# Kernel tuning notes

Hardware: AMD Instinct MI355X
Metric: run time of the kernel (lower is better)

The kernel has to match this reference:

```python
import math
import jax, jax.numpy as jnp
import numpy as np

NUM_HEADS = 16
QUERY_SIZE = 1024
SEQ = 2048
HEAD = QUERY_SIZE // NUM_HEADS  # qk_size = vo_size = 64


def setup_inputs() -> dict:
    key = jax.random.key(0)
    ks = jax.random.split(key, 8)
    s = 0.02
    query = jax.random.normal(ks[0], (SEQ, QUERY_SIZE), jnp.float32)
    key_ = jax.random.normal(ks[1], (SEQ, QUERY_SIZE), jnp.float32)
    value = jax.random.normal(ks[2], (SEQ, QUERY_SIZE), jnp.float32)
    # causal mask (mask='causal' with state=None -> offset 0)
    mask = jnp.tril(jnp.ones((SEQ, SEQ), dtype=bool))
    Wq = jax.random.normal(ks[3], (QUERY_SIZE, QUERY_SIZE), jnp.float32) * s
    Wk = jax.random.normal(ks[4], (QUERY_SIZE, QUERY_SIZE), jnp.float32) * s
    Wv = jax.random.normal(ks[5], (QUERY_SIZE, QUERY_SIZE), jnp.float32) * s
    Wo = jax.random.normal(ks[6], (QUERY_SIZE, QUERY_SIZE), jnp.float32) * s
    return {"query": query, "key_": key_, "value": value, "mask": mask,
            "Wq": Wq, "Wk": Wk, "Wv": Wv, "Wo": Wo}


def reference(query, key_, value, mask, Wq, Wk, Wv, Wo):
    H, D = NUMS = NUM_HEADS, HEAD
    S = query.shape[0]
    inv_sqrt_d = 1.0 / math.sqrt(D)
    # per-token linear projections, split into heads: [S, H, D]
    q = (query @ Wq.T).reshape(S, H, D)
    k = (key_ @ Wk.T).reshape(S, H, D)
    v = (value @ Wv.T).reshape(S, H, D)
    # NOTE: original divides BOTH q and k by sqrt(d) (effective 1/d scaling)
    q = q * inv_sqrt_d
    k = k * inv_sqrt_d
    # logits per head: [H, S, S]
    logits = jnp.einsum('shd,Shd->hsS', q, k)
    logits = jnp.where(mask[None, :, :], logits, jnp.finfo(logits.dtype).min)
    # per-head GLOBAL max subtraction, softmax in fp32, cast back (faithful)
    m = jnp.max(logits, axis=(1, 2), keepdims=True)
    weights = jax.nn.softmax((logits - m).astype(jnp.float32), axis=-1).astype(query.dtype)
    attn = jnp.einsum('hsS,ShD->shD', weights, v).reshape(S, H * D)
    return attn @ Wo.T
```

## Files before the change

### kernel.cpp

```cpp
#include <hip/hip_runtime.h>
#include <hip/hip_bf16.h>

typedef __bf16 bf16_t;
typedef __bf16 bf16x8 __attribute__((ext_vector_type(8)));
typedef float f32x4 __attribute__((ext_vector_type(4)));

#define MFMA(A, B, C) __builtin_amdgcn_mfma_f32_16x16x32_bf16(A, B, C, 0, 0, 0)

#define GLL16(g, l) __builtin_amdgcn_global_load_lds(                      \
    (const __attribute__((address_space(1))) void*)(g),                    \
    (__attribute__((address_space(3))) void*)(l), 16, 0, 0)

__global__ __launch_bounds__(256) void cvt_all(
    const float* __restrict__ q, const float* __restrict__ k, const float* __restrict__ v,
    const float* __restrict__ wq, const float* __restrict__ wk,
    const float* __restrict__ wv, const float* __restrict__ wo,
    bf16_t* __restrict__ xq, bf16_t* __restrict__ xk, bf16_t* __restrict__ xv,
    bf16_t* __restrict__ ywq, bf16_t* __restrict__ ywk,
    bf16_t* __restrict__ ywv, bf16_t* __restrict__ ywo)
{
  const long gid = (long)blockIdx.x * 256 + threadIdx.x;
  const float* s; bf16_t* d; long off; float sc = 1.0f;
  if (gid < 262144)       { s = q;  d = xq;  off = gid; }
  else if (gid < 524288)  { s = k;  d = xk;  off = gid - 262144; }
  else if (gid < 786432)  { s = v;  d = xv;  off = gid - 524288; }
  else if (gid < 917504)  { s = wq; d = ywq; off = gid - 786432;  sc = 0.125f; }
  else if (gid < 1048576) { s = wk; d = ywk; off = gid - 917504;  sc = 0.125f; }
  else if (gid < 1179648) { s = wv; d = ywv; off = gid - 1048576; }
  else                    { s = wo; d = ywo; off = gid - 1179648; }
  const float* p = s + off * 8;
  float4 a = *(const float4*)p, b = *(const float4*)(p + 4);
  bf16x8 o;
  o[0] = (bf16_t)(a.x * sc); o[1] = (bf16_t)(a.y * sc);
  o[2] = (bf16_t)(a.z * sc); o[3] = (bf16_t)(a.w * sc);
  o[4] = (bf16_t)(b.x * sc); o[5] = (bf16_t)(b.y * sc);
  o[6] = (bf16_t)(b.z * sc); o[7] = (bf16_t)(b.w * sc);
  *(bf16x8*)(d + off * 8) = o;
}

__device__ __forceinline__ void gemm_core(const bf16_t* __restrict__ A,
                                          const bf16_t* __restrict__ W,
                                          int bm, int bn,
                                          bf16_t (&As)[2][128 * 64],
                                          bf16_t (&Bs)[2][64 * 64],
                                          f32x4 (&acc)[4][2])
{
  const int tid = threadIdx.x, lane = tid & 63, wave = tid >> 6;
  const int l15 = lane & 15, l4 = lane >> 4, l7 = l15 & 7;
  const int wm = (wave >> 1) * 64, wn = (wave & 1) * 32;

  auto stage = [&](int buf, int k0) {
#pragma unroll
    for (int i = 0; i < 4; ++i) {
      const int id = i * 256 + tid;
      const int row = id >> 3, cph = id & 7;
      GLL16(A + (size_t)(bm + row) * 1024 + k0 + 8 * (cph ^ (row & 7)),
            &As[buf][(i * 256 + wave * 64) * 8]);
    }
#pragma unroll
    for (int i = 0; i < 2; ++i) {
      const int id = i * 256 + tid;
      const int row = id >> 3, cph = id & 7;
      GLL16(W + (size_t)(bn + row) * 1024 + k0 + 8 * (cph ^ (row & 7)),
            &Bs[buf][(i * 256 + wave * 64) * 8]);
    }
  };

  stage(0, 0);
#pragma unroll
  for (int s = 0; s < 16; ++s) {
    if (s + 1 < 16) stage((s + 1) & 1, (s + 1) * 64);
    __syncthreads();
    const bf16_t* as = As[s & 1];
    const bf16_t* bs = Bs[s & 1];
#pragma unroll
    for (int ks = 0; ks < 2; ++ks) {
      bf16x8 af[4], bfr[2];
#pragma unroll
      for (int i = 0; i < 4; ++i)
        af[i] = *(const bf16x8*)(&as[(wm + i * 16 + l15) * 64 + 8 * ((ks * 4 + l4) ^ l7)]);
#pragma unroll
      for (int j = 0; j < 2; ++j)
        bfr[j] = *(const bf16x8*)(&bs[(wn + j * 16 + l15) * 64 + 8 * ((ks * 4 + l4) ^ l7)]);
#pragma unroll
      for (int i = 0; i < 4; ++i)
#pragma unroll
        for (int j = 0; j < 2; ++j)
          acc[i][j] = MFMA(af[i], bfr[j], acc[i][j]);
    }
    __syncthreads();
  }
}

__global__ __launch_bounds__(256) void gemm_qkv(
    const bf16_t* __restrict__ xq, const bf16_t* __restrict__ xk, const bf16_t* __restrict__ xv,
    const bf16_t* __restrict__ ywq, const bf16_t* __restrict__ ywk, const bf16_t* __restrict__ ywv,
    bf16_t* __restrict__ qo, bf16_t* __restrict__ ko, bf16_t* __restrict__ vt)
{
  __shared__ __align__(16) bf16_t As[2][128 * 64];
  __shared__ __align__(16) bf16_t Bs[2][64 * 64];
  const int z = blockIdx.z;
  const bf16_t* A = z == 0 ? xq : z == 1 ? xk : xv;
  const bf16_t* W = z == 0 ? ywq : z == 1 ? ywk : ywv;
  const int bm = blockIdx.x * 128, bn = blockIdx.y * 64;
  f32x4 acc[4][2] = {};
  gemm_core(A, W, bm, bn, As, Bs, acc);
  const int tid = threadIdx.x, lane = tid & 63, wave = tid >> 6;
  const int l15 = lane & 15, l4 = lane >> 4;
  const int wm = (wave >> 1) * 64, wn = (wave & 1) * 32;
  if (z < 2) {
    bf16_t* C = z == 0 ? qo : ko;
#pragma unroll
    for (int i = 0; i < 4; ++i)
#pragma unroll
      for (int j = 0; j < 2; ++j)
#pragma unroll
        for (int r = 0; r < 4; ++r)
          C[(size_t)(bm + wm + i * 16 + 4 * l4 + r) * 1024 + bn + wn + j * 16 + l15] =
              (bf16_t)acc[i][j][r];
  } else {
#pragma unroll
    for (int i = 0; i < 4; ++i)
#pragma unroll
      for (int j = 0; j < 2; ++j)
#pragma unroll
        for (int r = 0; r < 4; ++r)
          vt[(size_t)(bn + wn + j * 16 + l15) * 2048 + bm + wm + i * 16 + 4 * l4 + r] =
              (bf16_t)acc[i][j][r];
  }
}

__global__ __launch_bounds__(256) void gemm_out(
    const bf16_t* __restrict__ ctx, const bf16_t* __restrict__ ywo, float* __restrict__ out)
{
  __shared__ __align__(16) bf16_t As[2][128 * 64];
  __shared__ __align__(16) bf16_t Bs[2][64 * 64];
  const int bm = blockIdx.x * 128, bn = blockIdx.y * 64;
  f32x4 acc[4][2] = {};
  gemm_core(ctx, ywo, bm, bn, As, Bs, acc);
  const int tid = threadIdx.x, lane = tid & 63, wave = tid >> 6;
  const int l15 = lane & 15, l4 = lane >> 4;
  const int wm = (wave >> 1) * 64, wn = (wave & 1) * 32;
#pragma unroll
  for (int i = 0; i < 4; ++i)
#pragma unroll
    for (int j = 0; j < 2; ++j)
#pragma unroll
      for (int r = 0; r < 4; ++r)
        out[(size_t)(bm + wm + i * 16 + 4 * l4 + r) * 1024 + bn + wn + j * 16 + l15] =
            acc[i][j][r];
}

__global__ __launch_bounds__(512) void attn512(
    const bf16_t* __restrict__ Qb, const bf16_t* __restrict__ Kb,
    const bf16_t* __restrict__ Vt, bf16_t* __restrict__ Ctx)
{
  __shared__ __align__(16) bf16_t Ks[2][128 * 64];
  __shared__ __align__(16) bf16_t Vs[2][64 * 128];
  __shared__ __align__(16) bf16_t Ps[8][16 * 64];

  const int bid = blockIdx.x;
  const int h = 2 * (bid & 7) + ((bid >> 3) >> 4);
  const int jp = (bid >> 3) & 15;
  const int hoff = h * 64;
  const int tid = threadIdx.x;
  const int lane = tid & 63, wave = tid >> 6;
  const int g = wave & 3, kh = wave >> 2;
  const int l15 = lane & 15, l4 = lane >> 4;
  const int l7 = l15 & 7;

  const int qtA = jp, qtB = 31 - jp;
  const int qbA = qtA * 64, qbB = qtB * 64;
  const int nscA = qtA / 2 + 1, nscB = qtB / 2 + 1;

  const int qrA = qbA + g * 16 + l15, qrB = qbB + g * 16 + l15;
  bf16x8 qA0 = *(const bf16x8*)(Qb + (size_t)qrA * 1024 + hoff + 8 * l4);
  bf16x8 qA1 = *(const bf16x8*)(Qb + (size_t)qrA * 1024 + hoff + 32 + 8 * l4);
  bf16x8 qB0 = *(const bf16x8*)(Qb + (size_t)qrB * 1024 + hoff + 8 * l4);
  bf16x8 qB1 = *(const bf16x8*)(Qb + (size_t)qrB * 1024 + hoff + 32 + 8 * l4);

  f32x4 oA[4] = {}, oB[4] = {};
  float dA[4] = {0.f, 0.f, 0.f, 0.f}, dB[4] = {0.f, 0.f, 0.f, 0.f};

  bf16x8 rk[2], rv[2];
  auto issue = [&](int sc) {
    const int t0 = sc * 128;
#pragma unroll
    for (int i = 0; i < 2; ++i) {
      const int id = tid + 512 * i;
      const int kr = id >> 3, kc = id & 7;
      rk[i] = *(const bf16x8*)(Kb + (size_t)(t0 + kr) * 1024 + hoff + 8 * kc);
      const int vr = id >> 4, vc = id & 15;
      rv[i] = *(const bf16x8*)(Vt + (size_t)(hoff + vr) * 2048 + t0 + 8 * vc);
    }
  };
  auto commit = [&](int buf) {
#pragma unroll
    for (int i = 0; i < 2; ++i) {
      const int id = tid + 512 * i;
      const int kr = id >> 3, kc = id & 7;
      *(bf16x8*)(&Ks[buf][kr * 64 + 8 * (kc ^ (kr & 7))]) = rk[i];
      const int vr = id >> 4, vc = id & 15;
      *(bf16x8*)(&Vs[buf][vr * 128 + 8 * (vc ^ (vr & 7))]) = rv[i];
    }
  };

  auto process = [&](int sc, int cur, int qb, const bf16x8& q0, const bf16x8& q1,
                     f32x4 (&oacc)[4], float (&den)[4]) {
    if (128 * sc + 64 * kh > qb + g * 16 + 15) return;
    const int tb = 128 * sc + 64 * kh;
#pragma unroll
    for (int sub = 0; sub < 4; ++sub) {
      const int krow = 64 * kh + 16 * sub + l15;
      bf16x8 kf0 = *(const bf16x8*)(&Ks[cur][krow * 64 + 8 * (l4 ^ l7)]);
      bf16x8 kf1 = *(const bf16x8*)(&Ks[cur][krow * 64 + 8 * ((4 + l4) ^ l7)]);
      f32x4 sv = {};
      sv = MFMA(q0, kf0, sv);
      sv = MFMA(q1, kf1, sv);
      const int t = tb + 16 * sub + l15;
#pragma unroll
      for (int r = 0; r < 4; ++r) {
        const int qq = qb + g * 16 + 4 * l4 + r;
        const float p = (t <= qq) ? __expf(sv[r]) : 0.0f;
        const bf16_t pb = (bf16_t)p;
        den[r] += (float)pb;
        const int prow = 4 * l4 + r;
        const int pch = 2 * sub + (l15 >> 3);
        Ps[wave][prow * 64 + 8 * (pch ^ (prow & 7)) + l7] = pb;
      }
    }
    asm volatile("s_waitcnt lgkmcnt(0)" ::: "memory");
#pragma unroll
    for (int ks = 0; ks < 2; ++ks) {
      bf16x8 pf = *(const bf16x8*)(&Ps[wave][l15 * 64 + 8 * ((ks * 4 + l4) ^ l7)]);
#pragma unroll
      for (int db = 0; db < 4; ++db) {
        bf16x8 vf = *(const bf16x8*)(&Vs[cur][(db * 16 + l15) * 128 + 64 * kh + 8 * ((ks * 4 + l4) ^ l7)]);
        oacc[db] = MFMA(pf, vf, oacc[db]);
      }
    }
  };

  issue(0);
  commit(0);
  int cur = 0;
  for (int sc = 0; sc < nscB; ++sc) {
    const bool pre = (sc + 1 < nscB);
    if (pre) issue(sc + 1);
    __syncthreads();
    process(sc, cur, qbB, qB0, qB1, oB, dB);
    if (sc < nscA) process(sc, cur, qbA, qA0, qA1, oA, dA);
    if (pre) commit(cur ^ 1);
    cur ^= 1;
  }

  __syncthreads();
#pragma unroll
  for (int r = 0; r < 4; ++r)
#pragma unroll
    for (int m = 1; m < 16; m <<= 1) {
      dA[r] += __shfl_xor(dA[r], m, 64);
      dB[r] += __shfl_xor(dB[r], m, 64);
    }
  float* Os = (float*)(&Ks[0][0]);
  float* Ds = (float*)(&Vs[0][0]);
  if (kh == 1) {
#pragma unroll
    for (int r = 0; r < 4; ++r) {
      const int row = g * 16 + 4 * l4 + r;
#pragma unroll
      for (int db = 0; db < 4; ++db) {
        Os[(0 * 64 + row) * 64 + db * 16 + l15] = oA[db][r];
        Os[(1 * 64 + row) * 64 + db * 16 + l15] = oB[db][r];
      }
      if (l15 == 0) { Ds[0 * 64 + row] = dA[r]; Ds[1 * 64 + row] = dB[r]; }
    }
  }
  __syncthreads();
  if (kh == 0) {
#pragma unroll
    for (int r = 0; r < 4; ++r) {
      const int row = g * 16 + 4 * l4 + r;
      const float iA = 1.0f / (dA[r] + Ds[0 * 64 + row]);
      const float iB = 1.0f / (dB[r] + Ds[1 * 64 + row]);
#pragma unroll
      for (int db = 0; db < 4; ++db) {
        const float vA = oA[db][r] + Os[(0 * 64 + row) * 64 + db * 16 + l15];
        const float vB = oB[db][r] + Os[(1 * 64 + row) * 64 + db * 16 + l15];
        Ctx[(size_t)(qbA + row) * 1024 + hoff + db * 16 + l15] = (bf16_t)(vA * iA);
        Ctx[(size_t)(qbB + row) * 1024 + hoff + db * 16 + l15] = (bf16_t)(vB * iB);
      }
    }
  }
}

extern "C" void kernel_launch(void* const* d_in, const int* in_sizes, int n_in,
                              void* d_out, int out_size, void* d_ws, size_t ws_size,
                              hipStream_t stream)
{
  const float* query = (const float*)d_in[0];
  const float* key_  = (const float*)d_in[1];
  const float* value = (const float*)d_in[2];
  const float* Wq = (const float*)d_in[4];
  const float* Wk = (const float*)d_in[5];
  const float* Wv = (const float*)d_in[6];
  const float* Wo = (const float*)d_in[7];
  float* out = (float*)d_out;

  const size_t SE = (size_t)2048 * 1024, EE = (size_t)1024 * 1024;
  bf16_t* xq  = (bf16_t*)d_ws;
  bf16_t* xk  = xq + SE;
  bf16_t* xv  = xk + SE;
  bf16_t* wq  = xv + SE;
  bf16_t* wk  = wq + EE;
  bf16_t* wv  = wk + EE;
  bf16_t* wo  = wv + EE;
  bf16_t* qo  = wo + EE;
  bf16_t* ko  = qo + SE;
  bf16_t* vt  = ko + SE;
  bf16_t* ctx = vt + SE;

  cvt_all<<<5120, 256, 0, stream>>>(query, key_, value, Wq, Wk, Wv, Wo,
                                    xq, xk, xv, wq, wk, wv, wo);
  gemm_qkv<<<dim3(16, 16, 3), 256, 0, stream>>>(xq, xk, xv, wq, wk, wv, qo, ko, vt);
  attn512<<<256, 512, 0, stream>>>(qo, ko, vt, ctx);
  gemm_out<<<dim3(16, 16), 256, 0, stream>>>(ctx, wo, out);
}
```

Baseline: 72.08 us.

## Fuse fp32-to-bf16 conversion into GEMM loaders and add MFMA priority hints

Removes the separate conversion kernel. Both GEMMs now load fp32 activations and weights straight into registers, convert to bf16 (applying the 1/8 scale to Wq and Wk) and write swizzled tiles into LDS through a register-staged double buffer. This saves one kernel launch and a bf16 workspace round trip. The cost is that each GEMM now reads twice the global bytes and does its own conversions, and the GEMMs re-read the weights from every block. The attention kernel also gets s_setprio boosts around its MFMA sections, and its barrier moves ahead of the prefetch issue.

```diff
diff --git a/kernel.cpp b/kernel.cpp
--- a/kernel.cpp
+++ b/kernel.cpp
@@ -11,103 +11,91 @@
     (const __attribute__((address_space(1))) void*)(g),                    \
     (__attribute__((address_space(3))) void*)(l), 16, 0, 0)
 
-__global__ __launch_bounds__(256) void cvt_all(
-    const float* __restrict__ q, const float* __restrict__ k, const float* __restrict__ v,
-    const float* __restrict__ wq, const float* __restrict__ wk,
-    const float* __restrict__ wv, const float* __restrict__ wo,
-    bf16_t* __restrict__ xq, bf16_t* __restrict__ xk, bf16_t* __restrict__ xv,
-    bf16_t* __restrict__ ywq, bf16_t* __restrict__ ywk,
-    bf16_t* __restrict__ ywv, bf16_t* __restrict__ ywo)
-{
-  const long gid = (long)blockIdx.x * 256 + threadIdx.x;
-  const float* s; bf16_t* d; long off; float sc = 1.0f;
-  if (gid < 262144)       { s = q;  d = xq;  off = gid; }
-  else if (gid < 524288)  { s = k;  d = xk;  off = gid - 262144; }
-  else if (gid < 786432)  { s = v;  d = xv;  off = gid - 524288; }
-  else if (gid < 917504)  { s = wq; d = ywq; off = gid - 786432;  sc = 0.125f; }
-  else if (gid < 1048576) { s = wk; d = ywk; off = gid - 917504;  sc = 0.125f; }
-  else if (gid < 1179648) { s = wv; d = ywv; off = gid - 1048576; }
-  else                    { s = wo; d = ywo; off = gid - 1179648; }
-  const float* p = s + off * 8;
-  float4 a = *(const float4*)p, b = *(const float4*)(p + 4);
+static __device__ __forceinline__ bf16x8 cvt8p(const float4& a, const float4& b, float sc) {
   bf16x8 o;
   o[0] = (bf16_t)(a.x * sc); o[1] = (bf16_t)(a.y * sc);
   o[2] = (bf16_t)(a.z * sc); o[3] = (bf16_t)(a.w * sc);
   o[4] = (bf16_t)(b.x * sc); o[5] = (bf16_t)(b.y * sc);
   o[6] = (bf16_t)(b.z * sc); o[7] = (bf16_t)(b.w * sc);
-  *(bf16x8*)(d + off * 8) = o;
-}
-
-__device__ __forceinline__ void gemm_core(const bf16_t* __restrict__ A,
-                                          const bf16_t* __restrict__ W,
-                                          int bm, int bn,
-                                          bf16_t (&As)[2][128 * 64],
-                                          bf16_t (&Bs)[2][64 * 64],
-                                          f32x4 (&acc)[4][2])
-{
-  const int tid = threadIdx.x, lane = tid & 63, wave = tid >> 6;
-  const int l15 = lane & 15, l4 = lane >> 4, l7 = l15 & 7;
-  const int wm = (wave >> 1) * 64, wn = (wave & 1) * 32;
-
-  auto stage = [&](int buf, int k0) {
-#pragma unroll
-    for (int i = 0; i < 4; ++i) {
-      const int id = i * 256 + tid;
-      const int row = id >> 3, cph = id & 7;
-      GLL16(A + (size_t)(bm + row) * 1024 + k0 + 8 * (cph ^ (row & 7)),
-            &As[buf][(i * 256 + wave * 64) * 8]);
-    }
-#pragma unroll
-    for (int i = 0; i < 2; ++i) {
-      const int id = i * 256 + tid;
-      const int row = id >> 3, cph = id & 7;
-      GLL16(W + (size_t)(bn + row) * 1024 + k0 + 8 * (cph ^ (row & 7)),
-            &Bs[buf][(i * 256 + wave * 64) * 8]);
-    }
-  };
-
-  stage(0, 0);
-#pragma unroll
-  for (int s = 0; s < 16; ++s) {
-    if (s + 1 < 16) stage((s + 1) & 1, (s + 1) * 64);
-    __syncthreads();
-    const bf16_t* as = As[s & 1];
-    const bf16_t* bs = Bs[s & 1];
-#pragma unroll
-    for (int ks = 0; ks < 2; ++ks) {
-      bf16x8 af[4], bfr[2];
-#pragma unroll
-      for (int i = 0; i < 4; ++i)
-        af[i] = *(const bf16x8*)(&as[(wm + i * 16 + l15) * 64 + 8 * ((ks * 4 + l4) ^ l7)]);
-#pragma unroll
-      for (int j = 0; j < 2; ++j)
-        bfr[j] = *(const bf16x8*)(&bs[(wn + j * 16 + l15) * 64 + 8 * ((ks * 4 + l4) ^ l7)]);
-#pragma unroll
-      for (int i = 0; i < 4; ++i)
-#pragma unroll
-        for (int j = 0; j < 2; ++j)
-          acc[i][j] = MFMA(af[i], bfr[j], acc[i][j]);
-    }
-    __syncthreads();
-  }
+  return o;
 }
 
 __global__ __launch_bounds__(256) void gemm_qkv(
-    const bf16_t* __restrict__ xq, const bf16_t* __restrict__ xk, const bf16_t* __restrict__ xv,
-    const bf16_t* __restrict__ ywq, const bf16_t* __restrict__ ywk, const bf16_t* __restrict__ ywv,
+    const float* __restrict__ xq, const float* __restrict__ xk, const float* __restrict__ xv,
+    const float* __restrict__ Wq, const float* __restrict__ Wk, const float* __restrict__ Wv,
     bf16_t* __restrict__ qo, bf16_t* __restrict__ ko, bf16_t* __restrict__ vt)
 {
   __shared__ __align__(16) bf16_t As[2][128 * 64];
   __shared__ __align__(16) bf16_t Bs[2][64 * 64];
   const int z = blockIdx.z;
-  const bf16_t* A = z == 0 ? xq : z == 1 ? xk : xv;
-  const bf16_t* W = z == 0 ? ywq : z == 1 ? ywk : ywv;
+  const float* A = z == 0 ? xq : z == 1 ? xk : xv;
+  const float* W = z == 0 ? Wq : z == 1 ? Wk : Wv;
+  const float wsc = z < 2 ? 0.125f : 1.0f;
   const int bm = blockIdx.x * 128, bn = blockIdx.y * 64;
+  const int tid = threadIdx.x, lane = tid & 63, wave = tid >> 6;
+  const int l15 = lane & 15, l4 = lane >> 4, l7 = l15 & 7;
+  const int wm = (wave >> 1) * 64, wn = (wave & 1) * 32;
+
+  float4 ra[4][2], rb[2][2];
+  auto aload = [&](int k0) {
+#pragma unroll
+    for (int i = 0; i < 4; ++i) {
+      const int id = i * 256 + tid, row = id >> 3, c = id & 7;
+      const float* p = A + (size_t)(bm + row) * 1024 + k0 + 8 * c;
+      ra[i][0] = *(const float4*)p; ra[i][1] = *(const float4*)(p + 4);
+    }
+  };
+  auto bload = [&](int k0) {
+#pragma unroll
+    for (int i = 0; i < 2; ++i) {
+      const int id = i * 256 + tid, row = id >> 3, c = id & 7;
+      const float* p = W + (size_t)(bn + row) * 1024 + k0 + 8 * c;
+      rb[i][0] = *(const float4*)p; rb[i][1] = *(const float4*)(p + 4);
+    }
+  };
+  auto abwrite = [&](int buf) {
+#pragma unroll
+    for (int i = 0; i < 4; ++i) {
+      const int id = i * 256 + tid, row = id >> 3, c = id & 7;
+      *(bf16x8*)(&As[buf][row * 64 + 8 * (c ^ (row & 7))]) = cvt8p(ra[i][0], ra[i][1], 1.0f);
+    }
+#pragma unroll
+    for (int i = 0; i < 2; ++i) {
+      const int id = i * 256 + tid, row = id >> 3, c = id & 7;
+      *(bf16x8*)(&Bs[buf][row * 64 + 8 * (c ^ (row & 7))]) = cvt8p(rb[i][0], rb[i][1], wsc);
+    }
+  };
+
   f32x4 acc[4][2] = {};
-  gemm_core(A, W, bm, bn, As, Bs, acc);
-  const int tid = threadIdx.x, lane = tid & 63, wave = tid >> 6;
-  const int l15 = lane & 15, l4 = lane >> 4;
-  const int wm = (wave >> 1) * 64, wn = (wave & 1) * 32;
+  aload(0); bload(0);
+  abwrite(0);
+  aload(64); bload(64);
+#pragma unroll
+  for (int s = 0; s < 16; ++s) {
+    __syncthreads();
+    if (s + 1 < 16) {
+      abwrite((s + 1) & 1);
+      if (s + 2 < 16) { aload((s + 2) * 64); bload((s + 2) * 64); }
+    }
+    const bf16_t* as = As[s & 1];
+    const bf16_t* bs = Bs[s & 1];
+#pragma unroll
+    for (int ks = 0; ks < 2; ++ks) {
+      bf16x8 af[4], bfr[2];
+#pragma unroll
+      for (int i = 0; i < 4; ++i)
+        af[i] = *(const bf16x8*)(&as[(wm + i * 16 + l15) * 64 + 8 * ((ks * 4 + l4) ^ l7)]);
+#pragma unroll
+      for (int j = 0; j < 2; ++j)
+        bfr[j] = *(const bf16x8*)(&bs[(wn + j * 16 + l15) * 64 + 8 * ((ks * 4 + l4) ^ l7)]);
+#pragma unroll
+      for (int i = 0; i < 4; ++i)
+#pragma unroll
+        for (int j = 0; j < 2; ++j)
+          acc[i][j] = MFMA(af[i], bfr[j], acc[i][j]);
+    }
+  }
+
   if (z < 2) {
     bf16_t* C = z == 0 ? qo : ko;
 #pragma unroll
@@ -131,16 +119,70 @@
 }
 
 __global__ __launch_bounds__(256) void gemm_out(
-    const bf16_t* __restrict__ ctx, const bf16_t* __restrict__ ywo, float* __restrict__ out)
+    const bf16_t* __restrict__ ctx, const float* __restrict__ Wo, float* __restrict__ out)
 {
   __shared__ __align__(16) bf16_t As[2][128 * 64];
   __shared__ __align__(16) bf16_t Bs[2][64 * 64];
   const int bm = blockIdx.x * 128, bn = blockIdx.y * 64;
+  const int tid = threadIdx.x, lane = tid & 63, wave = tid >> 6;
+  const int l15 = lane & 15, l4 = lane >> 4, l7 = l15 & 7;
+  const int wm = (wave >> 1) * 64, wn = (wave & 1) * 32;
+
+  auto astage = [&](int buf, int k0) {
+#pragma unroll
+    for (int i = 0; i < 4; ++i) {
+      const int id = i * 256 + tid, row = id >> 3, cph = id & 7;
+      GLL16(ctx + (size_t)(bm + row) * 1024 + k0 + 8 * (cph ^ (row & 7)),
+            &As[buf][(i * 256 + wave * 64) * 8]);
+    }
+  };
+  float4 rb[2][2];
+  auto bload = [&](int k0) {
+#pragma unroll
+    for (int i = 0; i < 2; ++i) {
+      const int id = i * 256 + tid, row = id >> 3, c = id & 7;
+      const float* p = Wo + (size_t)(bn + row) * 1024 + k0 + 8 * c;
+      rb[i][0] = *(const float4*)p; rb[i][1] = *(const float4*)(p + 4);
+    }
+  };
+  auto bwrite = [&](int buf) {
+#pragma unroll
+    for (int i = 0; i < 2; ++i) {
+      const int id = i * 256 + tid, row = id >> 3, c = id & 7;
+      *(bf16x8*)(&Bs[buf][row * 64 + 8 * (c ^ (row & 7))]) = cvt8p(rb[i][0], rb[i][1], 1.0f);
+    }
+  };
+
   f32x4 acc[4][2] = {};
-  gemm_core(ctx, ywo, bm, bn, As, Bs, acc);
-  const int tid = threadIdx.x, lane = tid & 63, wave = tid >> 6;
-  const int l15 = lane & 15, l4 = lane >> 4;
-  const int wm = (wave >> 1) * 64, wn = (wave & 1) * 32;
+  astage(0, 0); bload(0);
+  bwrite(0);
+  bload(64);
+#pragma unroll
+  for (int s = 0; s < 16; ++s) {
+    __syncthreads();
+    if (s + 1 < 16) {
+      astage((s + 1) & 1, (s + 1) * 64);
+      bwrite((s + 1) & 1);
+      if (s + 2 < 16) bload((s + 2) * 64);
+    }
+    const bf16_t* as = As[s & 1];
+    const bf16_t* bs = Bs[s & 1];
+#pragma unroll
+    for (int ks = 0; ks < 2; ++ks) {
+      bf16x8 af[4], bfr[2];
+#pragma unroll
+      for (int i = 0; i < 4; ++i)
+        af[i] = *(const bf16x8*)(&as[(wm + i * 16 + l15) * 64 + 8 * ((ks * 4 + l4) ^ l7)]);
+#pragma unroll
+      for (int j = 0; j < 2; ++j)
+        bfr[j] = *(const bf16x8*)(&bs[(wn + j * 16 + l15) * 64 + 8 * ((ks * 4 + l4) ^ l7)]);
+#pragma unroll
+      for (int i = 0; i < 4; ++i)
+#pragma unroll
+        for (int j = 0; j < 2; ++j)
+          acc[i][j] = MFMA(af[i], bfr[j], acc[i][j]);
+    }
+  }
 #pragma unroll
   for (int i = 0; i < 4; ++i)
 #pragma unroll
@@ -214,9 +256,11 @@
       const int krow = 64 * kh + 16 * sub + l15;
       bf16x8 kf0 = *(const bf16x8*)(&Ks[cur][krow * 64 + 8 * (l4 ^ l7)]);
       bf16x8 kf1 = *(const bf16x8*)(&Ks[cur][krow * 64 + 8 * ((4 + l4) ^ l7)]);
+      __builtin_amdgcn_s_setprio(1);
       f32x4 sv = {};
       sv = MFMA(q0, kf0, sv);
       sv = MFMA(q1, kf1, sv);
+      __builtin_amdgcn_s_setprio(0);
       const int t = tb + 16 * sub + l15;
 #pragma unroll
       for (int r = 0; r < 4; ++r) {
@@ -230,6 +274,7 @@
       }
     }
     asm volatile("s_waitcnt lgkmcnt(0)" ::: "memory");
+    __builtin_amdgcn_s_setprio(1);
 #pragma unroll
     for (int ks = 0; ks < 2; ++ks) {
       bf16x8 pf = *(const bf16x8*)(&Ps[wave][l15 * 64 + 8 * ((ks * 4 + l4) ^ l7)]);
@@ -239,6 +284,7 @@
         oacc[db] = MFMA(pf, vf, oacc[db]);
       }
     }
+    __builtin_amdgcn_s_setprio(0);
   };
 
   issue(0);
@@ -246,8 +292,8 @@
   int cur = 0;
   for (int sc = 0; sc < nscB; ++sc) {
     const bool pre = (sc + 1 < nscB);
+    __syncthreads();
     if (pre) issue(sc + 1);
-    __syncthreads();
     process(sc, cur, qbB, qB0, qB1, oB, dB);
     if (sc < nscA) process(sc, cur, qbA, qA0, qA1, oA, dA);
     if (pre) commit(cur ^ 1);
@@ -307,22 +353,13 @@
   const float* Wo = (const float*)d_in[7];
   float* out = (float*)d_out;
 
-  const size_t SE = (size_t)2048 * 1024, EE = (size_t)1024 * 1024;
-  bf16_t* xq  = (bf16_t*)d_ws;
-  bf16_t* xk  = xq + SE;
-  bf16_t* xv  = xk + SE;
-  bf16_t* wq  = xv + SE;
-  bf16_t* wk  = wq + EE;
-  bf16_t* wv  = wk + EE;
-  bf16_t* wo  = wv + EE;
-  bf16_t* qo  = wo + EE;
+  const size_t SE = (size_t)2048 * 1024;
+  bf16_t* qo  = (bf16_t*)d_ws;
   bf16_t* ko  = qo + SE;
   bf16_t* vt  = ko + SE;
   bf16_t* ctx = vt + SE;
 
-  cvt_all<<<5120, 256, 0, stream>>>(query, key_, value, Wq, Wk, Wv, Wo,
-                                    xq, xk, xv, wq, wk, wv, wo);
-  gemm_qkv<<<dim3(16, 16, 3), 256, 0, stream>>>(xq, xk, xv, wq, wk, wv, qo, ko, vt);
+  gemm_qkv<<<dim3(16, 16, 3), 256, 0, stream>>>(query, key_, value, Wq, Wk, Wv, qo, ko, vt);
   attn512<<<256, 512, 0, stream>>>(qo, ko, vt, ctx);
-  gemm_out<<<dim3(16, 16), 256, 0, stream>>>(ctx, wo, out);
-}
+  gemm_out<<<dim3(16, 16), 256, 0, stream>>>(ctx, Wo, out);
+}
```

Result: slower. 80.61 us (+11.8%).
